# Performance work log

Hardware: AMD Instinct MI355X
Metric: run time of the kernel (lower is better)

## Reference

```python
import jax, jax.numpy as jnp
import numpy as np

B, N, M, A, P, W = 8, 4096, 4, 32, 4, 16


def setup_inputs() -> dict:
    key = jax.random.key(0)
    k_x, k_adj, k_w, k_b = jax.random.split(key, 4)
    x = jax.random.normal(k_x, (B, N, M, A), dtype=jnp.float32)
    adj = jax.random.uniform(k_adj, (B, N, N), dtype=jnp.float32)
    # kaiming-uniform-style init: bound = sqrt(6 / fan_in), fan_in = A * W (per torch conv fan-in heuristic); exact scale irrelevant for correctness
    bound = float(np.sqrt(6.0 / (A * W)))
    weight = jax.random.uniform(k_w, (M, P, A, W), dtype=jnp.float32, minval=-bound, maxval=bound)
    bias = jax.random.uniform(k_b, (1, 1, P, W), dtype=jnp.float32)
    return {"x": x, "adj": adj, "weight": weight, "bias": bias}


def _normalize(adj):
    # mx = adj + I (self loops)
    mx = adj + jnp.eye(adj.shape[1], dtype=adj.dtype)[None, :, :]
    rowsum = jnp.sum(mx, axis=2)                      # [B, N]
    r_inv = 1.0 / rowsum
    r_inv = jnp.where(jnp.isinf(r_inv), 0.0, r_inv)
    # diag_embed(r_inv) @ mx == row-scaling; same math, O(N^2) instead of O(N^3)
    return mx * r_inv[:, :, None]


def reference(x, adj, weight, bias):
    # per-modal feature transform: [B,N,M,A] x [M,P,A,W] -> [B,N,P,W]
    h = jnp.einsum('bnma,mpaw->bnpw', x, weight)
    adj_n = _normalize(adj)
    # weighted aggregation over neighbors: [B,N,N] x [B,N,P,W] -> [B,N,P,W]
    out = jax.nn.relu(jnp.einsum('bnc,bcpw->bnpw', adj_n, h))
    return out + bias
```

## Files before the change

### kernel.cpp

```cpp
#include <hip/hip_runtime.h>
#include <hip/hip_bf16.h>
#include <math.h>


typedef __bf16 bf16_t;
typedef __bf16 bf16x8 __attribute__((ext_vector_type(8)));
typedef float f32x4 __attribute__((ext_vector_type(4)));

__global__ __launch_bounds__(256) void feat_kernel(
    const float* __restrict__ x, const float* __restrict__ weight,
    bf16_t* __restrict__ Ht)
{
  __shared__ float xs[64 * 129];
  const int tid = threadIdx.x;
  const int node0 = blockIdx.x * 64;

  const float* xb = x + (size_t)node0 * 128;
  #pragma unroll
  for (int it = 0; it < 8; ++it) {
    int g = (it * 256 + tid) * 4;
    float4 v = *(const float4*)(xb + g);
    int nd = g >> 7, ma = g & 127;
    float* d = &xs[nd * 129 + ma];
    d[0] = v.x; d[1] = v.y; d[2] = v.z; d[3] = v.w;
  }
  __syncthreads();

  const int lane = tid & 63;
  const int p = __builtin_amdgcn_readfirstlane(tid >> 6);

  float acc[16];
  #pragma unroll
  for (int w = 0; w < 16; ++w) acc[w] = 0.f;

  #pragma unroll 4
  for (int ma = 0; ma < 128; ++ma) {
    float xv = xs[lane * 129 + ma];
    const float* wrow = weight + (((size_t)(ma >> 5) * 4 + p) * 32 + (ma & 31)) * 16;
    #pragma unroll
    for (int w = 0; w < 16; ++w) acc[w] += xv * wrow[w];
  }

  const int node_g = node0 + lane;
  const int b = node_g >> 12;
  const int n = node_g & 4095;
  bf16_t* hbase = Ht + ((size_t)b * 64 + p * 16) * 4096 + n;
  #pragma unroll
  for (int w = 0; w < 16; ++w) hbase[(size_t)w * 4096] = (bf16_t)acc[w];
}

__global__ __launch_bounds__(256) void agg_kernel(
    const float* __restrict__ adj, const bf16_t* __restrict__ Ht,
    const float* __restrict__ bias, float* __restrict__ out)
{
  const int bid = blockIdx.x;
  const int b  = bid & 7;
  const int rt = bid >> 3;
  const int tid  = threadIdx.x;
  const int wv   = tid >> 6;
  const int lane = tid & 63;
  const int l = lane & 15;
  const int q = lane >> 4;

  const int rowg = rt * 64 + wv * 16 + l;
  const float*  arow = adj + ((size_t)b * 4096 + rowg) * 4096;
  const bf16_t* hb   = Ht + (size_t)b * 64 * 4096;

  f32x4 acc0 = {0.f,0.f,0.f,0.f}, acc1 = acc0, acc2 = acc0, acc3 = acc0;
  float rsum = 0.f;
  const int diag_k0 = rt * 64;

  for (int k0 = 0; k0 < 4096; k0 += 64) {
    float av[16];
    *(float4*)&av[0]  = *(const float4*)(arow + k0 + q * 8);
    *(float4*)&av[4]  = *(const float4*)(arow + k0 + q * 8 + 4);
    *(float4*)&av[8]  = *(const float4*)(arow + k0 + 32 + q * 8);
    *(float4*)&av[12] = *(const float4*)(arow + k0 + 32 + q * 8 + 4);

    if (k0 == diag_k0) {
      int d  = rowg - k0;
      int e0 = d - q * 8;
      if (e0 >= 0 && e0 < 8)  av[e0] += 1.f;
      int e1 = d - 32 - q * 8;
      if (e1 >= 0 && e1 < 8)  av[8 + e1] += 1.f;
    }

    #pragma unroll
    for (int j = 0; j < 16; ++j) rsum += av[j];

    bf16x8 af0, af1;
    #pragma unroll
    for (int j = 0; j < 8; ++j) { af0[j] = (bf16_t)av[j]; af1[j] = (bf16_t)av[8 + j]; }

    const bf16_t* hk = hb + (size_t)l * 4096 + k0 + q * 8;
    acc0 = __builtin_amdgcn_mfma_f32_16x16x32_bf16(af0, *(const bf16x8*)(hk),                 acc0, 0, 0, 0);
    acc0 = __builtin_amdgcn_mfma_f32_16x16x32_bf16(af1, *(const bf16x8*)(hk + 32),            acc0, 0, 0, 0);
    acc1 = __builtin_amdgcn_mfma_f32_16x16x32_bf16(af0, *(const bf16x8*)(hk + 16*4096),       acc1, 0, 0, 0);
    acc1 = __builtin_amdgcn_mfma_f32_16x16x32_bf16(af1, *(const bf16x8*)(hk + 16*4096 + 32),  acc1, 0, 0, 0);
    acc2 = __builtin_amdgcn_mfma_f32_16x16x32_bf16(af0, *(const bf16x8*)(hk + 32*4096),       acc2, 0, 0, 0);
    acc2 = __builtin_amdgcn_mfma_f32_16x16x32_bf16(af1, *(const bf16x8*)(hk + 32*4096 + 32),  acc2, 0, 0, 0);
    acc3 = __builtin_amdgcn_mfma_f32_16x16x32_bf16(af0, *(const bf16x8*)(hk + 48*4096),       acc3, 0, 0, 0);
    acc3 = __builtin_amdgcn_mfma_f32_16x16x32_bf16(af1, *(const bf16x8*)(hk + 48*4096 + 32),  acc3, 0, 0, 0);
  }

  rsum += __shfl_xor(rsum, 16);
  rsum += __shfl_xor(rsum, 32);
  float ri = 1.0f / rsum;
  if (isinf(ri)) ri = 0.f;

  float bv0 = bias[l], bv1 = bias[16 + l], bv2 = bias[32 + l], bv3 = bias[48 + l];

  float* orow = out + ((size_t)b * 4096 + rt * 64 + wv * 16) * 64;
  #pragma unroll
  for (int i = 0; i < 4; ++i) {
    int row = q * 4 + i;
    float riv = __shfl(ri, row);
    float* o = orow + (size_t)row * 64 + l;
    o[0]  = fmaxf(acc0[i] * riv, 0.f) + bv0;
    o[16] = fmaxf(acc1[i] * riv, 0.f) + bv1;
    o[32] = fmaxf(acc2[i] * riv, 0.f) + bv2;
    o[48] = fmaxf(acc3[i] * riv, 0.f) + bv3;
  }
}

extern "C" void kernel_launch(void* const* d_in, const int* in_sizes, int n_in,
                              void* d_out, int out_size, void* d_ws, size_t ws_size,
                              hipStream_t stream) {
  const float* x      = (const float*)d_in[0];
  const float* adj    = (const float*)d_in[1];
  const float* weight = (const float*)d_in[2];
  const float* bias   = (const float*)d_in[3];
  float* out = (float*)d_out;

  bf16_t* Ht = (bf16_t*)d_ws;

  feat_kernel<<<512, 256, 0, stream>>>(x, weight, Ht);
  agg_kernel<<<512, 256, 0, stream>>>(adj, Ht, bias, out);
}
```

Before: 785.0 us.

## Split K across waves in aggregation kernel with LDS reduction and register prefetch

Each block now handles 16 rows instead of 64, and its four waves each take a quarter of the K dimension. Partial accumulators and row sums are reduced through shared memory, which raises the grid from 512 to 2048 blocks for more parallelism and latency hiding. The adj loads are also software-prefetched one iteration ahead in registers. In exchange it adds an LDS reduction and a barrier. Each block's H reads now cover a K quarter for only 16 rows, so H is re-read across four times as many blocks.

Measured after the change: 789.8 us. About the same (+0.6%).

```diff
diff --git a/kernel.cpp b/kernel.cpp
--- a/kernel.cpp
+++ b/kernel.cpp
@@ -53,6 +53,9 @@
     const float* __restrict__ adj, const bf16_t* __restrict__ Ht,
     const float* __restrict__ bias, float* __restrict__ out)
 {
+  __shared__ float accLds[4][64][17];
+  __shared__ float rsumLds[4][16];
+
   const int bid = blockIdx.x;
   const int b  = bid & 7;
   const int rt = bid >> 3;
@@ -62,27 +65,39 @@
   const int l = lane & 15;
   const int q = lane >> 4;
 
-  const int rowg = rt * 64 + wv * 16 + l;
-  const float*  arow = adj + ((size_t)b * 4096 + rowg) * 4096;
+  const int rowg = rt * 16 + l;
+  const float*  arow = adj + ((size_t)b * 4096 + rowg) * 4096 + wv * 1024;
   const bf16_t* hb   = Ht + (size_t)b * 64 * 4096;
 
   f32x4 acc0 = {0.f,0.f,0.f,0.f}, acc1 = acc0, acc2 = acc0, acc3 = acc0;
   float rsum = 0.f;
-  const int diag_k0 = rt * 64;
 
-  for (int k0 = 0; k0 < 4096; k0 += 64) {
+  const int c  = rowg - wv * 1024;
+  const bool own_diag = (c >= 0) && (c < 1024);
+  const int td = c >> 6;
+  const int dd = c & 63;
+
+  float4 p0 = *(const float4*)(arow + q * 8);
+  float4 p1 = *(const float4*)(arow + q * 8 + 4);
+  float4 p2 = *(const float4*)(arow + 32 + q * 8);
+  float4 p3 = *(const float4*)(arow + 32 + q * 8 + 4);
+
+  for (int t = 0; t < 16; ++t) {
     float av[16];
-    *(float4*)&av[0]  = *(const float4*)(arow + k0 + q * 8);
-    *(float4*)&av[4]  = *(const float4*)(arow + k0 + q * 8 + 4);
-    *(float4*)&av[8]  = *(const float4*)(arow + k0 + 32 + q * 8);
-    *(float4*)&av[12] = *(const float4*)(arow + k0 + 32 + q * 8 + 4);
+    *(float4*)&av[0]  = p0;  *(float4*)&av[4]  = p1;
+    *(float4*)&av[8]  = p2;  *(float4*)&av[12] = p3;
 
-    if (k0 == diag_k0) {
-      int d  = rowg - k0;
-      int e0 = d - q * 8;
-      if (e0 >= 0 && e0 < 8)  av[e0] += 1.f;
-      int e1 = d - 32 - q * 8;
-      if (e1 >= 0 && e1 < 8)  av[8 + e1] += 1.f;
+    if (t < 15) {
+      const float* an = arow + (t + 1) * 64;
+      p0 = *(const float4*)(an + q * 8);
+      p1 = *(const float4*)(an + q * 8 + 4);
+      p2 = *(const float4*)(an + 32 + q * 8);
+      p3 = *(const float4*)(an + 32 + q * 8 + 4);
+    }
+
+    if (own_diag && t == td) {
+      int e0 = dd - q * 8;       if (e0 >= 0 && e0 < 8) av[e0]     += 1.f;
+      int e1 = dd - 32 - q * 8;  if (e1 >= 0 && e1 < 8) av[8 + e1] += 1.f;
     }
 
     #pragma unroll
@@ -92,7 +107,7 @@
     #pragma unroll
     for (int j = 0; j < 8; ++j) { af0[j] = (bf16_t)av[j]; af1[j] = (bf16_t)av[8 + j]; }
 
-    const bf16_t* hk = hb + (size_t)l * 4096 + k0 + q * 8;
+    const bf16_t* hk = hb + (size_t)l * 4096 + wv * 1024 + t * 64 + q * 8;
     acc0 = __builtin_amdgcn_mfma_f32_16x16x32_bf16(af0, *(const bf16x8*)(hk),                 acc0, 0, 0, 0);
     acc0 = __builtin_amdgcn_mfma_f32_16x16x32_bf16(af1, *(const bf16x8*)(hk + 32),            acc0, 0, 0, 0);
     acc1 = __builtin_amdgcn_mfma_f32_16x16x32_bf16(af0, *(const bf16x8*)(hk + 16*4096),       acc1, 0, 0, 0);
@@ -105,21 +120,35 @@
 
   rsum += __shfl_xor(rsum, 16);
   rsum += __shfl_xor(rsum, 32);
-  float ri = 1.0f / rsum;
+  if (q == 0) rsumLds[wv][l] = rsum;
+
+  #pragma unroll
+  for (int i = 0; i < 4; ++i) {
+    accLds[wv][lane][i]      = acc0[i];
+    accLds[wv][lane][4 + i]  = acc1[i];
+    accLds[wv][lane][8 + i]  = acc2[i];
+    accLds[wv][lane][12 + i] = acc3[i];
+  }
+  __syncthreads();
+
+  float sum[4];
+  #pragma unroll
+  for (int i = 0; i < 4; ++i)
+    sum[i] = accLds[0][lane][wv*4 + i] + accLds[1][lane][wv*4 + i]
+           + accLds[2][lane][wv*4 + i] + accLds[3][lane][wv*4 + i];
+
+  float rtot = rsumLds[0][l] + rsumLds[1][l] + rsumLds[2][l] + rsumLds[3][l];
+  float ri = 1.0f / rtot;
   if (isinf(ri)) ri = 0.f;
 
-  float bv0 = bias[l], bv1 = bias[16 + l], bv2 = bias[32 + l], bv3 = bias[48 + l];
+  float bv = bias[wv * 16 + l];
 
-  float* orow = out + ((size_t)b * 4096 + rt * 64 + wv * 16) * 64;
+  float* orow = out + ((size_t)b * 4096 + rt * 16) * 64 + wv * 16;
   #pragma unroll
   for (int i = 0; i < 4; ++i) {
     int row = q * 4 + i;
     float riv = __shfl(ri, row);
-    float* o = orow + (size_t)row * 64 + l;
-    o[0]  = fmaxf(acc0[i] * riv, 0.f) + bv0;
-    o[16] = fmaxf(acc1[i] * riv, 0.f) + bv1;
-    o[32] = fmaxf(acc2[i] * riv, 0.f) + bv2;
-    o[48] = fmaxf(acc3[i] * riv, 0.f) + bv3;
+    orow[(size_t)row * 64 + l] = fmaxf(sum[i] * riv, 0.f) + bv;
   }
 }
 
@@ -135,5 +164,5 @@
   bf16_t* Ht = (bf16_t*)d_ws;
 
   feat_kernel<<<512, 256, 0, stream>>>(x, weight, Ht);
-  agg_kernel<<<512, 256, 0, stream>>>(adj, Ht, bias, out);
+  agg_kernel<<<2048, 256, 0, stream>>>(adj, Ht, bias, out);
 }
```
